# Kernel tuning notes

Hardware: AMD Instinct MI355X
Metric: run time of the kernel (lower is better)

The kernel has to match this reference:

```python
import jax, jax.numpy as jnp
import numpy as np

B, C, Ci, H, W = 4, 256, 128, 64, 64  # batch, in_channels, inter_channels, spatial
BN_EPS = 1e-5


def setup_inputs() -> dict:
    key = jax.random.key(0)
    ks = jax.random.split(key, 8)
    s = (2.0 / C) ** 0.5  # kaiming fan_in std for 1x1 conv over C inputs
    return {
        "a": jax.random.normal(ks[0], (B, C, H, W), jnp.float32),
        "b": jax.random.normal(ks[1], (B, C, H, W), jnp.float32),
        "theta_w": jax.random.normal(ks[2], (Ci, C), jnp.float32) * s,
        "theta_b": jnp.zeros((Ci,), jnp.float32),
        "phi_w": jax.random.normal(ks[3], (Ci, C), jnp.float32) * s,
        "phi_b": jnp.zeros((Ci,), jnp.float32),
        "g_w": jax.random.normal(ks[4], (Ci, C), jnp.float32) * s,
        "g_b": jnp.zeros((Ci,), jnp.float32),
        "W_w": jax.random.normal(ks[5], (C, Ci), jnp.float32) * (2.0 / Ci) ** 0.5,
        "bn_gamma": jnp.ones((C,), jnp.float32),
        "bn_beta": jnp.zeros((C,), jnp.float32),
        "bn_mean": jnp.zeros((C,), jnp.float32),
        "bn_var": jnp.ones((C,), jnp.float32),
    }


def _conv1x1(x, w, bias=None):
    # x: [B,Cin,H,W], w: [Cout,Cin] -> [B,Cout,H,W]
    y = jnp.einsum("oc,bchw->bohw", w, x)
    if bias is not None:
        y = y + bias[None, :, None, None]
    return y


def reference(a, b, theta_w, theta_b, phi_w, phi_b, g_w, g_b, W_w,
              bn_gamma, bn_beta, bn_mean, bn_var):
    Bsz, _, h, w = a.shape
    n = h * w
    theta_a = _conv1x1(a, theta_w, theta_b).reshape(Bsz, Ci, n).transpose(0, 2, 1)  # [B,N,Ci]
    phi_b_ = _conv1x1(b, phi_w, phi_b).reshape(Bsz, Ci, n)                          # [B,Ci,N]
    f = jnp.einsum("bnc,bcm->bnm", theta_a, phi_b_) / n                             # [B,N,N]
    g_b_ = _conv1x1(b, g_w, g_b).reshape(Bsz, Ci, n).transpose(0, 2, 1)             # [B,N,Ci]
    y = jnp.einsum("bnm,bmc->bnc", f, g_b_)                                         # [B,N,Ci]
    y = y.transpose(0, 2, 1).reshape(Bsz, Ci, h, w)
    wy = _conv1x1(y, W_w)                                                           # no bias
    inv = jax.lax.rsqrt(bn_var + BN_EPS)
    out = (wy - bn_mean[None, :, None, None]) * (bn_gamma * inv)[None, :, None, None] \
          + bn_beta[None, :, None, None]
    return out
```

## Files before the change

### kernel.cpp

```cpp
#include <hip/hip_runtime.h>
#include <hip/hip_bf16.h>

#define NSP 4096
#define CCH 256
#define CIN 128
#define BN_EPS 1e-5f

typedef __bf16 bf16x8 __attribute__((ext_vector_type(8)));
typedef __bf16 bf16x4 __attribute__((ext_vector_type(4)));
typedef float f32x4 __attribute__((ext_vector_type(4)));
typedef unsigned short u16x8 __attribute__((ext_vector_type(8)));


__device__ __forceinline__ float4 fetch_tr(const float* __restrict__ A, int lda, int m0,
                                           int k0, int tid) {
  const int r = tid >> 2, kq = (tid & 3) << 2;
  return *(const float4*)(A + (size_t)(m0 + r) * lda + k0 + kq);
}
__device__ __forceinline__ void stash_tr(float (*As)[68], float4 v, int tid) {
  const int r = tid >> 2, kq = (tid & 3) << 2;
  As[kq + 0][r] = v.x; As[kq + 1][r] = v.y; As[kq + 2][r] = v.z; As[kq + 3][r] = v.w;
}
__device__ __forceinline__ float4 fetch_dir(const float* __restrict__ B, int ldb, int k0,
                                            int n0, int tid) {
  const int kr = tid >> 4, nq = (tid & 15) << 2;
  return *(const float4*)(B + (size_t)(k0 + kr) * ldb + n0 + nq);
}
__device__ __forceinline__ void stash_dir(float (*Bs)[68], float4 v, int tid) {
  const int kr = tid >> 4, nq = (tid & 15) << 2;
  *(float4*)(&Bs[kr][nq]) = v;
}

__device__ __forceinline__ void mm16(const float (*As)[68], const float (*Bs)[68],
                                     float acc[4][4], int ty, int tx) {
#pragma unroll
  for (int kk = 0; kk < 16; ++kk) {
    const float4 av = *(const float4*)(&As[kk][ty << 2]);
    const float4 bv = *(const float4*)(&Bs[kk][tx << 2]);
    const float ar[4] = {av.x, av.y, av.z, av.w};
    const float br[4] = {bv.x, bv.y, bv.z, bv.w};
#pragma unroll
    for (int i = 0; i < 4; ++i)
#pragma unroll
      for (int j = 0; j < 4; ++j) acc[i][j] += ar[i] * br[j];
  }
}

__device__ __forceinline__ float wave_reduce(float v) {
#pragma unroll
  for (int off = 32; off; off >>= 1) v += __shfl_down(v, off);
  return v;
}

__global__ __launch_bounds__(256) void prep_kernel(
    const float* __restrict__ bin, const float* __restrict__ a,
    const float* __restrict__ W_w, const float* __restrict__ g_w,
    const float* __restrict__ phi_w, const float* __restrict__ theta_w,
    const float* __restrict__ phi_b, const float* __restrict__ theta_b,
    const float* __restrict__ g_b,
    __bf16* __restrict__ bhi, __bf16* __restrict__ blo,
    float* __restrict__ srow,
    float* __restrict__ Wg, __bf16* __restrict__ Wghi, __bf16* __restrict__ Wglo,
    __bf16* __restrict__ PTthi, __bf16* __restrict__ PTtlo,
    __bf16* __restrict__ at,
    float* __restrict__ vb_g, float* __restrict__ vpt, float* __restrict__ wgb,
    float* __restrict__ dvec) {
  __shared__ float smem[64 * 68];
  const int idx = blockIdx.x;
  const int t = threadIdx.x;
  const int wave = t >> 6, lane = t & 63;
  if (idx < 1024) {
    const int row = idx;
    const float* src = bin + (size_t)row * NSP + t * 16;
    float sum = 0.f;
    unsigned short h16[16], l16[16];
#pragma unroll
    for (int i = 0; i < 4; ++i) {
      const float4 v = *(const float4*)(src + i * 4);
      const float vv[4] = {v.x, v.y, v.z, v.w};
      sum += v.x + v.y + v.z + v.w;
#pragma unroll
      for (int e = 0; e < 4; ++e) {
        const unsigned u = __float_as_uint(vv[e]);
        h16[i * 4 + e] = (unsigned short)(u >> 16);
        const float hf = __uint_as_float(u & 0xffff0000u);
        l16[i * 4 + e] = (unsigned short)(__float_as_uint(vv[e] - hf) >> 16);
      }
    }
    unsigned short* dh = (unsigned short*)bhi + (size_t)row * NSP + t * 16;
    unsigned short* dl = (unsigned short*)blo + (size_t)row * NSP + t * 16;
    *(u16x8*)dh = *(u16x8*)&h16[0];
    *(u16x8*)(dh + 8) = *(u16x8*)&h16[8];
    *(u16x8*)dl = *(u16x8*)&l16[0];
    *(u16x8*)(dl + 8) = *(u16x8*)&l16[8];
#pragma unroll
    for (int off = 32; off; off >>= 1) sum += __shfl_down(sum, off);
    if (lane == 0) smem[wave] = sum;
    __syncthreads();
    if (t == 0) srow[row] = smem[0] + smem[1] + smem[2] + smem[3];
  } else if (idx < 2048) {
    const int p = idx - 1024;
    const int n0 = (p & 63) * 64, c0 = ((p >> 6) & 3) * 64, b = p >> 8;
    float (*tile)[68] = (float(*)[68])smem;
    const int cr = t >> 4, nq = (t & 15) << 2;
    const float* src = a + ((size_t)(b * CCH + c0)) * NSP + n0;
#pragma unroll
    for (int s = 0; s < 4; ++s) {
      const float4 v = *(const float4*)(src + (size_t)(cr + s * 16) * NSP + nq);
      *(float4*)&tile[cr + s * 16][nq] = v;
    }
    __syncthreads();
    const int n = t >> 2, cq = (t & 3) << 4;
    __bf16 outv[16];
#pragma unroll
    for (int i = 0; i < 16; ++i) outv[i] = (__bf16)tile[cq + i][n];
    __bf16* dst = at + ((size_t)(b * NSP + n0 + n)) * CCH + c0 + cq;
    *(bf16x8*)dst = *(bf16x8*)&outv[0];
    *(bf16x8*)(dst + 8) = *(bf16x8*)&outv[8];
  } else if (idx < 2080) {
    const int p = idx - 2048;
    const int zsel = p >> 4, rem = p & 15;
    const int m0 = (rem >> 2) * 64, n0 = (rem & 3) * 64;
    float (*As)[68] = (float(*)[68])smem;
    float (*Bs)[68] = (float(*)[68])(smem + 16 * 68);
    const int ty = t >> 4, tx = t & 15;
    float acc[4][4] = {};
    if (zsel == 0) {
      float4 ar = fetch_tr(W_w, CIN, m0, 0, t);
      float4 br = fetch_dir(g_w, CCH, 0, n0, t);
      for (int kt = 0; kt < 8; ++kt) {
        stash_tr(As, ar, t); stash_dir(Bs, br, t);
        __syncthreads();
        if (kt < 7) { ar = fetch_tr(W_w, CIN, m0, (kt + 1) * 16, t);
                      br = fetch_dir(g_w, CCH, (kt + 1) * 16, n0, t); }
        mm16(As, Bs, acc, ty, tx);
        __syncthreads();
      }
#pragma unroll
      for (int i = 0; i < 4; ++i) {
        const size_t off = (size_t)(m0 + (ty << 2) + i) * 256 + n0 + (tx << 2);
        *(float4*)(Wg + off) = make_float4(acc[i][0], acc[i][1], acc[i][2], acc[i][3]);
        __bf16 h4[4], l4[4];
#pragma unroll
        for (int j = 0; j < 4; ++j) {
          const __bf16 h = (__bf16)acc[i][j];
          h4[j] = h; l4[j] = (__bf16)(acc[i][j] - (float)h);
        }
        *(bf16x4*)(Wghi + off) = *(bf16x4*)h4;
        *(bf16x4*)(Wglo + off) = *(bf16x4*)l4;
      }
    } else {
      float4 ar = fetch_dir(theta_w, CCH, 0, m0, t);
      float4 br = fetch_dir(phi_w, CCH, 0, n0, t);
      for (int kt = 0; kt < 8; ++kt) {
        stash_dir(As, ar, t); stash_dir(Bs, br, t);
        __syncthreads();
        if (kt < 7) { ar = fetch_dir(theta_w, CCH, (kt + 1) * 16, m0, t);
                      br = fetch_dir(phi_w, CCH, (kt + 1) * 16, n0, t); }
        mm16(As, Bs, acc, ty, tx);
        __syncthreads();
      }
#pragma unroll
      for (int i = 0; i < 4; ++i) {
        const size_t off = (size_t)(m0 + (ty << 2) + i) * 256 + n0 + (tx << 2);
        __bf16 h4[4], l4[4];
#pragma unroll
        for (int j = 0; j < 4; ++j) {
          const __bf16 h = (__bf16)acc[i][j];
          h4[j] = h; l4[j] = (__bf16)(acc[i][j] - (float)h);
        }
        *(bf16x4*)(PTthi + off) = *(bf16x4*)h4;
        *(bf16x4*)(PTtlo + off) = *(bf16x4*)l4;
      }
    }
  } else if (idx == 2080) {
    float* tb_s = smem;
    float* pb_s = smem + 128;
    if (t < 128) { tb_s[t] = theta_b[t]; pb_s[t] = phi_b[t]; }
    __syncthreads();
    float acc = 0.f;
#pragma unroll 8
    for (int i = 0; i < 128; ++i) acc += phi_w[(size_t)i * 256 + t] * tb_s[i];
    vb_g[t] = acc;
    if (t < 64) {
      float pv = pb_s[t] * tb_s[t] + pb_s[t + 64] * tb_s[t + 64];
      pv = wave_reduce(pv);
      if (t == 0) dvec[0] = pv;
    }
  } else if (idx == 2081) {
    float* pb_s = smem;
    if (t < 128) pb_s[t] = phi_b[t];
    __syncthreads();
    float acc = 0.f;
#pragma unroll 8
    for (int i = 0; i < 128; ++i) acc += pb_s[i] * theta_w[(size_t)i * 256 + t];
    vpt[t] = acc;
  } else {
    const int p = idx - 2082;
    float* gb_s = smem;
    if (t < 128) gb_s[t] = g_b[t];
    __syncthreads();
    const float2 gv = *(const float2*)&gb_s[lane * 2];
    for (int i = 0; i < 16; ++i) {
      const int o = p * 64 + wave * 16 + i;
      const float2 r = *(const float2*)(W_w + (size_t)o * 128 + lane * 2);
      float v = fmaf(r.x, gv.x, r.y * gv.y);
      v = wave_reduce(v);
      if (lane == 0) wgb[o] = v;
    }
  }
}

__global__ __launch_bounds__(256) void gram_kernel(
    const __bf16* __restrict__ bhi, const __bf16* __restrict__ blo,
    float* __restrict__ Gpart) {
  const int idx = blockIdx.x;
  const int t = threadIdx.x;
  const int wave = t >> 6, lane = t & 63;
  const int jt = idx & 3, it = (idx >> 2) & 3;
  const int z = idx >> 4, batch = z >> 4, kc = z & 15;
  const int m = lane & 15, q = lane >> 4;
  const size_t base = (size_t)batch * CCH * NSP;
  const __bf16* ah_p = bhi + base + (size_t)(it * 64 + wave * 16 + m) * NSP + kc * 256 + q * 8;
  const __bf16* al_p = blo + base + (size_t)(it * 64 + wave * 16 + m) * NSP + kc * 256 + q * 8;
  const __bf16* bh_p = bhi + base + (size_t)(jt * 64 + m) * NSP + kc * 256 + q * 8;
  const __bf16* bl_p = blo + base + (size_t)(jt * 64 + m) * NSP + kc * 256 + q * 8;
  f32x4 acc[4] = {};
#pragma unroll
  for (int ks = 0; ks < 8; ++ks) {
    const int k = ks * 32;
    const bf16x8 ah = *(const bf16x8*)(ah_p + k);
    const bf16x8 al = *(const bf16x8*)(al_p + k);
#pragma unroll
    for (int t4 = 0; t4 < 4; ++t4) {
      const bf16x8 bh = *(const bf16x8*)(bh_p + (size_t)t4 * 16 * NSP + k);
      const bf16x8 bl = *(const bf16x8*)(bl_p + (size_t)t4 * 16 * NSP + k);
      acc[t4] = __builtin_amdgcn_mfma_f32_16x16x32_bf16(ah, bh, acc[t4], 0, 0, 0);
      acc[t4] = __builtin_amdgcn_mfma_f32_16x16x32_bf16(ah, bl, acc[t4], 0, 0, 0);
      acc[t4] = __builtin_amdgcn_mfma_f32_16x16x32_bf16(al, bh, acc[t4], 0, 0, 0);
    }
  }
  float* Gp = Gpart + ((size_t)(kc * 4 + batch)) * 65536;
#pragma unroll
  for (int t4 = 0; t4 < 4; ++t4)
#pragma unroll
    for (int r = 0; r < 4; ++r)
      Gp[(size_t)(it * 64 + wave * 16 + q * 4 + r) * 256 + jt * 64 + t4 * 16 + m] =
          acc[t4][r];
}

__global__ __launch_bounds__(256) void redw2_kernel(
    const float* __restrict__ Gpart, const float* __restrict__ vb_g,
    float* __restrict__ t2_g, const float* __restrict__ srow,
    const float* __restrict__ Wg,
    const __bf16* __restrict__ Wghi, const __bf16* __restrict__ Wglo,
    const __bf16* __restrict__ PTthi, const __bf16* __restrict__ PTtlo,
    __bf16* __restrict__ W2hi, __bf16* __restrict__ W2lo,
    float* __restrict__ Wgs, float* __restrict__ sPTv, float* __restrict__ dvec) {
  const int blk = blockIdx.x;
  const int t = threadIdx.x;
  const int wave = t >> 6, lane = t & 63;
  __shared__ __bf16 Gsh[16][264], Gsl[16][264];
  __shared__ float lds[256];
  if (blk < 64) {
    const int b = blk >> 4, nt = blk & 15;
    const int rr = t >> 4;
    const int c0 = (t & 15) * 16;
    f32x4 s[4] = {};
#pragma unroll
    for (int p = 0; p < 16; ++p) {
      const float* src = Gpart + (((size_t)(p * 4 + b)) << 16) +
                         (size_t)(nt * 16 + rr) * 256 + c0;
#pragma unroll
      for (int e = 0; e < 4; ++e) s[e] += *(const f32x4*)(src + e * 4);
    }
    {
      float part = 0.f;
#pragma unroll
      for (int e = 0; e < 4; ++e) {
        const float4 vv = *(const float4*)(vb_g + c0 + e * 4);
        part += s[e][0] * vv.x + s[e][1] * vv.y + s[e][2] * vv.z + s[e][3] * vv.w;
      }
#pragma unroll
      for (int off = 8; off; off >>= 1) part += __shfl_down(part, off);
      if ((t & 15) == 0) t2_g[b * 256 + nt * 16 + rr] = part;
    }
    __bf16 h8[16], l8[16];
#pragma unroll
    for (int e = 0; e < 16; ++e) {
      const float x = s[e >> 2][e & 3];
      const __bf16 h = (__bf16)x;
      h8[e] = h; l8[e] = (__bf16)(x - (float)h);
    }
    *(bf16x8*)&Gsh[rr][c0] = *(bf16x8*)&h8[0];
    *(bf16x8*)&Gsh[rr][c0 + 8] = *(bf16x8*)&h8[8];
    *(bf16x8*)&Gsl[rr][c0] = *(bf16x8*)&l8[0];
    *(bf16x8*)&Gsl[rr][c0 + 8] = *(bf16x8*)&l8[8];
    __syncthreads();
    const int m = lane & 15, q = lane >> 4;
    f32x4 acc[4] = {};
#pragma unroll
    for (int ks = 0; ks < 8; ++ks) {
      const int k = ks * 32 + q * 8;
      const bf16x8 bh = *(const bf16x8*)&Gsh[m][k];
      const bf16x8 bl = *(const bf16x8*)&Gsl[m][k];
#pragma unroll
      for (int i = 0; i < 4; ++i) {
        const int mt = i * 4 + wave;
        const bf16x8 ah = *(const bf16x8*)(Wghi + (size_t)(mt * 16 + m) * 256 + k);
        const bf16x8 al = *(const bf16x8*)(Wglo + (size_t)(mt * 16 + m) * 256 + k);
        acc[i] = __builtin_amdgcn_mfma_f32_16x16x32_bf16(ah, bh, acc[i], 0, 0, 0);
        acc[i] = __builtin_amdgcn_mfma_f32_16x16x32_bf16(ah, bl, acc[i], 0, 0, 0);
        acc[i] = __builtin_amdgcn_mfma_f32_16x16x32_bf16(al, bh, acc[i], 0, 0, 0);
      }
    }
#pragma unroll
    for (int i = 0; i < 4; ++i) {
      const int mt = i * 4 + wave;
#pragma unroll
      for (int r = 0; r < 4; ++r) {
        const size_t off = ((size_t)b << 16) + (size_t)(mt * 16 + q * 4 + r) * 256 +
                           nt * 16 + m;
        const float v = acc[i][r];
        const __bf16 h = (__bf16)v;
        W2hi[off] = h;
        W2lo[off] = (__bf16)(v - (float)h);
      }
    }
  } else {
    const int p = blk - 64;
    const int b = p >> 4, seg = p & 15;
    lds[t] = srow[b * 256 + t];
    __syncthreads();
    const float4 sv = *(const float4*)&lds[lane * 4];
    for (int i = wave; i < 16; i += 4) {
      const int o = seg * 16 + i;
      const float4 r = *(const float4*)(Wg + (size_t)o * 256 + lane * 4);
      float v = fmaf(r.x, sv.x, fmaf(r.y, sv.y, fmaf(r.z, sv.z, r.w * sv.w)));
      v = wave_reduce(v);
      if (lane == 0) Wgs[b * 256 + o] = v;
    }
    for (int i = wave; i < 16; i += 4) {
      const int c = seg * 16 + i;
      const bf16x4 ph = *(const bf16x4*)(PTthi + (size_t)c * 256 + lane * 4);
      const bf16x4 pl = *(const bf16x4*)(PTtlo + (size_t)c * 256 + lane * 4);
      const float svv[4] = {sv.x, sv.y, sv.z, sv.w};
      float v = 0.f;
#pragma unroll
      for (int e = 0; e < 4; ++e) v += ((float)ph[e] + (float)pl[e]) * svv[e];
      v = wave_reduce(v);
      if (lane == 0) sPTv[b * 256 + c] = v;
    }
    if (seg == 0 && wave == 0) {
      const float4 vbv = *(const float4*)(vb_g + lane * 4);
      float v = fmaf(vbv.x, sv.x, fmaf(vbv.y, sv.y, fmaf(vbv.z, sv.z, vbv.w * sv.w)));
      v = wave_reduce(v);
      if (lane == 0) dvec[1 + b] = v;
    }
  }
}

__global__ __launch_bounds__(256) void wout_mfma_kernel(
    const __bf16* __restrict__ W2hi, const __bf16* __restrict__ W2lo,
    const __bf16* __restrict__ PTthi, const __bf16* __restrict__ PTtlo,
    const float* __restrict__ Wgs, const float* __restrict__ sPT,
    const float* __restrict__ wgb, const float* __restrict__ vpt,
    const float* __restrict__ Wg, const float* __restrict__ t2_g,
    const float* __restrict__ dvec,
    const float* __restrict__ bn_gamma, const float* __restrict__ bn_beta,
    const float* __restrict__ bn_mean, const float* __restrict__ bn_var,
    __bf16* __restrict__ Whi, __bf16* __restrict__ Wlo,
    float* __restrict__ bias_out) {
  const int blk = blockIdx.x;
  const int t = threadIdx.x;
  const int wave = t >> 6, lane = t & 63;
  if (blk < 64) {
    const int batch = blk >> 4, nt = blk & 15;
    const int m = lane & 15, q = lane >> 4;
    const __bf16* bh_p = PTthi + (size_t)(nt * 16 + m) * 256;
    const __bf16* bl_p = PTtlo + (size_t)(nt * 16 + m) * 256;
    const __bf16* w2h = W2hi + (size_t)batch * 65536;
    const __bf16* w2l = W2lo + (size_t)batch * 65536;
    f32x4 acc[4] = {};
#pragma unroll
    for (int ks = 0; ks < 8; ++ks) {
      const int k = ks * 32 + q * 8;
      const bf16x8 bh = *(const bf16x8*)(bh_p + k);
      const bf16x8 bl = *(const bf16x8*)(bl_p + k);
#pragma unroll
      for (int i = 0; i < 4; ++i) {
        const int mt = i * 4 + wave;
        const bf16x8 ah = *(const bf16x8*)(w2h + (size_t)(mt * 16 + m) * 256 + k);
        const bf16x8 al = *(const bf16x8*)(w2l + (size_t)(mt * 16 + m) * 256 + k);
        acc[i] = __builtin_amdgcn_mfma_f32_16x16x32_bf16(ah, bh, acc[i], 0, 0, 0);
        acc[i] = __builtin_amdgcn_mfma_f32_16x16x32_bf16(ah, bl, acc[i], 0, 0, 0);
        acc[i] = __builtin_amdgcn_mfma_f32_16x16x32_bf16(al, bh, acc[i], 0, 0, 0);
      }
    }
    const float invN = 1.0f / 4096.0f;
    const int c = nt * 16 + m;
    const float vpt_c = vpt[c];
    const float sPT_c = sPT[batch * 256 + c];
#pragma unroll
    for (int i = 0; i < 4; ++i) {
      const int mt = i * 4 + wave;
#pragma unroll
      for (int r = 0; r < 4; ++r) {
        const int o = mt * 16 + q * 4 + r;
        const float sc = bn_gamma[o] * rsqrtf(bn_var[o] + BN_EPS);
        const float w = sc * ((acc[i][r] + Wgs[batch * 256 + o] * vpt_c + wgb[o] * sPT_c) * invN +
                              wgb[o] * vpt_c);
        const size_t off = (size_t)batch * 65536 + (size_t)o * 256 + c;
        const __bf16 h = (__bf16)w;
        Whi[off] = h;
        Wlo[off] = (__bf16)(w - (float)h);
      }
    }
  } else {
    const int p = blk - 64;
    const int b = p >> 2, quarter = p & 3;
    __shared__ float t2s[256];
    t2s[t] = t2_g[b * 256 + t];
    __syncthreads();
    const float d1 = dvec[0], d2 = dvec[1 + b];
    const float invN = 1.0f / 4096.0f;
    const float4 tv = *(const float4*)&t2s[lane * 4];
    for (int it = 0; it < 16; ++it) {
      const int o = quarter * 64 + wave * 16 + it;
      const float4 r = *(const float4*)(Wg + (size_t)o * 256 + lane * 4);
      float v = fmaf(r.x, tv.x, fmaf(r.y, tv.y, fmaf(r.z, tv.z, r.w * tv.w)));
      v = wave_reduce(v);
      if (lane == 0) {
        const float bias_full = (v + Wgs[b * 256 + o] * d1 +
                                 wgb[o] * (d2 + 4096.0f * d1)) * invN;
        const float sc = bn_gamma[o] * rsqrtf(bn_var[o] + BN_EPS);
        bias_out[b * 256 + o] = sc * (bias_full - bn_mean[o]) + bn_beta[o];
      }
    }
  }
}

__global__ __launch_bounds__(256) void out_mfma_kernel(const __bf16* __restrict__ Whi,
                                                       const __bf16* __restrict__ Wlo,
                                                       const __bf16* __restrict__ at,
                                                       const float* __restrict__ bias_out,
                                                       float* __restrict__ out) {
  const int nt = blockIdx.x, mt = blockIdx.y, b = blockIdx.z;
  const int wave = threadIdx.x >> 6, lane = threadIdx.x & 63;
  const int m = lane & 15, q = lane >> 4;
  const int o = mt * 64 + wave * 16 + m;
  const __bf16* wh = Whi + (size_t)b * 65536 + (size_t)o * 256;
  const __bf16* wl = Wlo + (size_t)b * 65536 + (size_t)o * 256;
  const __bf16* atb = at + ((size_t)b * NSP + nt * 64) * CCH;
  f32x4 acc[4] = {};
#pragma unroll
  for (int ks = 0; ks < 8; ++ks) {
    const int k = ks * 32 + q * 8;
    const bf16x8 ah = *(const bf16x8*)(wh + k);
    const bf16x8 al = *(const bf16x8*)(wl + k);
#pragma unroll
    for (int t4 = 0; t4 < 4; ++t4) {
      const bf16x8 bh = *(const bf16x8*)(atb + (size_t)(t4 * 16 + m) * 256 + k);
      acc[t4] = __builtin_amdgcn_mfma_f32_16x16x32_bf16(ah, bh, acc[t4], 0, 0, 0);
      acc[t4] = __builtin_amdgcn_mfma_f32_16x16x32_bf16(al, bh, acc[t4], 0, 0, 0);
    }
  }
  float* ob = out + (size_t)b * CCH * NSP;
#pragma unroll
  for (int r = 0; r < 4; ++r) {
    const int orow = mt * 64 + wave * 16 + q * 4 + r;
    const float bo = bias_out[b * 256 + orow];
#pragma unroll
    for (int t4 = 0; t4 < 4; ++t4)
      ob[(size_t)orow * NSP + nt * 64 + t4 * 16 + m] = acc[t4][r] + bo;
  }
}

extern "C" void kernel_launch(void* const* d_in, const int* in_sizes, int n_in,
                              void* d_out, int out_size, void* d_ws, size_t ws_size,
                              hipStream_t stream) {
  (void)in_sizes; (void)n_in; (void)out_size; (void)ws_size;
  const float* a       = (const float*)d_in[0];
  const float* bI      = (const float*)d_in[1];
  const float* theta_w = (const float*)d_in[2];
  const float* theta_b = (const float*)d_in[3];
  const float* phi_w   = (const float*)d_in[4];
  const float* phi_b   = (const float*)d_in[5];
  const float* g_w     = (const float*)d_in[6];
  const float* g_b     = (const float*)d_in[7];
  const float* W_w     = (const float*)d_in[8];
  const float* bn_gamma= (const float*)d_in[9];
  const float* bn_beta = (const float*)d_in[10];
  const float* bn_mean = (const float*)d_in[11];
  const float* bn_var  = (const float*)d_in[12];
  float* out = (float*)d_out;
  float* ws  = (float*)d_ws;

  float* Gpart    = ws;
  float* srow     = ws + 4194304;
  float* Wg       = ws + 4195328;
  float* bias_out = ws + 4260864;
  float* Wgs      = ws + 4261888;
  float* sPTv     = ws + 4262912;
  float* wgb      = ws + 4263936;
  float* vpt      = ws + 4264192;
  float* vb_g     = ws + 4264448;
  float* t2_g     = ws + 4264704;
  float* dvec     = ws + 4265728;
  __bf16* at    = (__bf16*)(ws + 4265984);
  __bf16* Wghi  = (__bf16*)(ws + 6363136);
  __bf16* Wglo  = (__bf16*)(ws + 6395904);
  __bf16* PTthi = (__bf16*)(ws + 6428672);
  __bf16* PTtlo = (__bf16*)(ws + 6461440);
  __bf16* W2hi  = (__bf16*)(ws + 6494208);
  __bf16* W2lo  = (__bf16*)(ws + 6625280);
  __bf16* Whi   = (__bf16*)(ws + 6756352);
  __bf16* Wlo   = (__bf16*)(ws + 6887424);
  __bf16* bhi   = (__bf16*)(ws + 7018496);
  __bf16* blo   = (__bf16*)(ws + 9115648);

  prep_kernel<<<dim3(2086), dim3(256), 0, stream>>>(bI, a, W_w, g_w, phi_w, theta_w,
                                                    phi_b, theta_b, g_b,
                                                    bhi, blo, srow, Wg, Wghi, Wglo,
                                                    PTthi, PTtlo, at,
                                                    vb_g, vpt, wgb, dvec);
  gram_kernel<<<dim3(1024), dim3(256), 0, stream>>>(bhi, blo, Gpart);
  redw2_kernel<<<dim3(128), dim3(256), 0, stream>>>(Gpart, vb_g, t2_g, srow, Wg,
                                                    Wghi, Wglo, PTthi, PTtlo,
                                                    W2hi, W2lo, Wgs, sPTv, dvec);
  wout_mfma_kernel<<<dim3(80), dim3(256), 0, stream>>>(W2hi, W2lo, PTthi, PTtlo,
                                                       Wgs, sPTv, wgb, vpt, Wg, t2_g,
                                                       dvec, bn_gamma, bn_beta, bn_mean,
                                                       bn_var, Whi, Wlo, bias_out);
  out_mfma_kernel<<<dim3(64, 4, 4), dim3(256), 0, stream>>>(Whi, Wlo, at, bias_out, out);
}
```

Measured before the change: 203.6 us.

## Stage gram kernel operands through double-buffered LDS via direct global-to-LDS loads

The gram kernel used to read its bf16 hi/lo operands straight from global memory for every MFMA, so each B tile was re-read by all four waves. It now copies 64x32 hi/lo tiles of A and B into double-buffered shared memory with global_load_lds, using an XOR swizzle to limit bank conflicts, and prefetches the next k-step while the current one computes. This trades redundant global traffic and load latency for LDS use and one barrier per k-step. The gram kernel is only one of several kernels, so the overall gain is bounded by its share of the runtime.

```diff
diff --git a/kernel.cpp b/kernel.cpp
--- a/kernel.cpp
+++ b/kernel.cpp
@@ -10,6 +10,9 @@
 typedef __bf16 bf16x4 __attribute__((ext_vector_type(4)));
 typedef float f32x4 __attribute__((ext_vector_type(4)));
 typedef unsigned short u16x8 __attribute__((ext_vector_type(8)));
+
+typedef const __attribute__((address_space(1))) unsigned int gu32;
+typedef __attribute__((address_space(3))) unsigned int lu32;
 
 
 __device__ __forceinline__ float4 fetch_tr(const float* __restrict__ A, int lda, int m0,
@@ -214,31 +217,54 @@
 __global__ __launch_bounds__(256) void gram_kernel(
     const __bf16* __restrict__ bhi, const __bf16* __restrict__ blo,
     float* __restrict__ Gpart) {
+  __shared__ __bf16 At[2][64][64];
+  __shared__ __bf16 Bt[2][64][64];
   const int idx = blockIdx.x;
   const int t = threadIdx.x;
   const int wave = t >> 6, lane = t & 63;
   const int jt = idx & 3, it = (idx >> 2) & 3;
   const int z = idx >> 4, batch = z >> 4, kc = z & 15;
   const int m = lane & 15, q = lane >> 4;
-  const size_t base = (size_t)batch * CCH * NSP;
-  const __bf16* ah_p = bhi + base + (size_t)(it * 64 + wave * 16 + m) * NSP + kc * 256 + q * 8;
-  const __bf16* al_p = blo + base + (size_t)(it * 64 + wave * 16 + m) * NSP + kc * 256 + q * 8;
-  const __bf16* bh_p = bhi + base + (size_t)(jt * 64 + m) * NSP + kc * 256 + q * 8;
-  const __bf16* bl_p = blo + base + (size_t)(jt * 64 + m) * NSP + kc * 256 + q * 8;
+  const size_t rowbase = (size_t)batch * CCH;
+  const int colbase = kc * 256;
+  const int rseg = lane >> 3, ch = lane & 7;
+  const int u = ch ^ rseg;
+  const int h = u >> 2, j = u & 3;
+  const __bf16* gsrc = h ? blo : bhi;
+
+  auto stage = [&](int ph, int ks) {
+#pragma unroll
+    for (int c = 0; c < 4; ++c) {
+      const int s = wave * 4 + c;
+      const int isB = s >> 3;
+      const int kb = s & 7;
+      const int grow = (isB ? jt : it) * 64 + kb * 8 + rseg;
+      const __bf16* gp = gsrc + (rowbase + (size_t)grow) * NSP +
+                         colbase + ks * 32 + j * 8;
+      const __bf16* lp = isB ? &Bt[ph][kb * 8][0] : &At[ph][kb * 8][0];
+      __builtin_amdgcn_global_load_lds((gu32*)(const void*)gp,
+                                       (lu32*)(void*)lp, 16, 0, 0);
+    }
+  };
+
   f32x4 acc[4] = {};
-#pragma unroll
+  const int chA = q ^ (m & 7);
+  stage(0, 0);
+  int ph = 0;
   for (int ks = 0; ks < 8; ++ks) {
-    const int k = ks * 32;
-    const bf16x8 ah = *(const bf16x8*)(ah_p + k);
-    const bf16x8 al = *(const bf16x8*)(al_p + k);
+    __syncthreads();
+    if (ks < 7) stage(ph ^ 1, ks + 1);
+    const bf16x8 ah = *(const bf16x8*)&At[ph][wave * 16 + m][chA * 8];
+    const bf16x8 al = *(const bf16x8*)&At[ph][wave * 16 + m][(chA ^ 4) * 8];
 #pragma unroll
     for (int t4 = 0; t4 < 4; ++t4) {
-      const bf16x8 bh = *(const bf16x8*)(bh_p + (size_t)t4 * 16 * NSP + k);
-      const bf16x8 bl = *(const bf16x8*)(bl_p + (size_t)t4 * 16 * NSP + k);
+      const bf16x8 bh = *(const bf16x8*)&Bt[ph][t4 * 16 + m][chA * 8];
+      const bf16x8 bl = *(const bf16x8*)&Bt[ph][t4 * 16 + m][(chA ^ 4) * 8];
       acc[t4] = __builtin_amdgcn_mfma_f32_16x16x32_bf16(ah, bh, acc[t4], 0, 0, 0);
       acc[t4] = __builtin_amdgcn_mfma_f32_16x16x32_bf16(ah, bl, acc[t4], 0, 0, 0);
       acc[t4] = __builtin_amdgcn_mfma_f32_16x16x32_bf16(al, bh, acc[t4], 0, 0, 0);
     }
+    ph ^= 1;
   }
   float* Gp = Gpart + ((size_t)(kc * 4 + batch)) * 65536;
 #pragma unroll
```

Measured after the change: 184.1 us. -9.5%, faster.
